# Performance work log

Measured on AMD Instinct MI355X. Metric: run time of the kernel, lower is better.

The kernel has to match this reference:

```python
import jax, jax.numpy as jnp
import numpy as np

N, E, G = 50000, 300000, 256
H, LAT, VOCAB = 256, 64, 100
BN_EPS = 1e-5


def _bn(x, gamma, beta):
    # BatchNorm1d in training mode: per-feature batch mean / biased var
    mu = x.mean(axis=0)
    var = x.var(axis=0)
    return gamma * (x - mu) * jax.lax.rsqrt(var + BN_EPS) + beta


def _gconv(x, edge_attr, src, dst):
    # message: softplus(x_j + e), aggregate: scatter-add to dst, update: +(1+eps)*x with eps=0
    m = jax.nn.softplus(x[src] + edge_attr)          # [E, H]
    agg = jax.ops.segment_sum(m, dst, num_segments=N)  # [N, H]
    return agg + x


def setup_inputs() -> dict:
    key = jax.random.key(0)
    ks = jax.random.split(key, 16)
    inp = {
        "node_type": jax.random.randint(ks[0], (N,), 0, VOCAB),
        "edge_type": jax.random.randint(ks[1], (E,), 0, VOCAB),
        "edge_index": jax.random.randint(ks[2], (2, E), 0, N),
        "batch": jnp.sort(jax.random.randint(ks[3], (N,), 0, G)),
        "node_emb_w": jax.random.normal(ks[4], (VOCAB, H), jnp.float32),
        "edge_emb_w": jax.random.normal(ks[5], (VOCAB, H), jnp.float32),
        "g1": jnp.ones((H,), jnp.float32), "b1": jnp.zeros((H,), jnp.float32),
        "g2": jnp.ones((H,), jnp.float32), "b2": jnp.zeros((H,), jnp.float32),
        "g3": jnp.ones((H,), jnp.float32), "b3": jnp.zeros((H,), jnp.float32),
        "go1": jnp.ones((H,), jnp.float32), "bo1": jnp.zeros((H,), jnp.float32),
        "go2": jnp.ones((H // 2,), jnp.float32), "bo2": jnp.zeros((H // 2,), jnp.float32),
        "W1": jax.random.normal(ks[6], (2 * H, H), jnp.float32) * (2 * H) ** -0.5,
        "B1": jnp.zeros((H,), jnp.float32),
        "W2": jax.random.normal(ks[7], (H, H // 2), jnp.float32) * H ** -0.5,
        "B2": jnp.zeros((H // 2,), jnp.float32),
        "W3": jax.random.normal(ks[8], (H // 2, 2 * LAT), jnp.float32) * (H // 2) ** -0.5,
        "B3": jnp.zeros((2 * LAT,), jnp.float32),
    }
    return inp


def reference(node_type, edge_type, edge_index, batch,
              node_emb_w, edge_emb_w,
              g1, b1, g2, b2, g3, b3, go1, bo1, go2, bo2,
              W1, B1, W2, B2, W3, B3):
    act = jax.nn.softplus
    src, dst = edge_index[0], edge_index[1]
    h = node_emb_w[node_type]            # [N, H]
    e = edge_emb_w[edge_type]            # [E, H]
    h = act(_bn(_gconv(h, e, src, dst), g1, b1))
    h = act(_bn(_gconv(h, e, src, dst), g2, b2))
    h = _bn(_gconv(h, e, src, dst), g3, b3)
    h_global = jax.ops.segment_sum(h, batch, num_segments=G)  # [G, H]
    feat = jnp.concatenate([h, h_global[batch]], axis=-1)     # [N, 2H]
    feat = act(_bn(feat @ W1 + B1, go1, bo1))
    feat = act(_bn(feat @ W2 + B2, go2, bo2))
    out = feat @ W3 + B3                                      # [N, 2*LAT]
    return out[:, :LAT], out[:, LAT:]
```

## Files before the change

kernel.cpp:

```cpp
#include <hip/hip_runtime.h>
#include <hip/hip_bf16.h>

namespace {

constexpr int N = 50000;
constexpr int E = 300000;
constexpr int G = 256;
constexpr int H = 256;
constexpr float EPS = 1e-5f;
constexpr int NB = (N + 255) / 256;
constexpr int POOL_S = 16;
constexpr int GBL = 256;
constexpr int NVB = N / 16;
constexpr float LOG2E = 1.4426950408889634f;
constexpr float LN2   = 0.6931471805599453f;

typedef unsigned short u16;
typedef __attribute__((ext_vector_type(8))) short bf16x8;
typedef __attribute__((ext_vector_type(4))) float f32x4;

__device__ __forceinline__ float expnabs(float z){
  float r; asm("v_exp_f32 %0, -abs(%1)" : "=v"(r) : "v"(z)); return r;
}
__device__ __forceinline__ float log2f_(float x){
  float r; asm("v_log_f32 %0, %1" : "=v"(r) : "v"(x)); return r;
}
__device__ __forceinline__ float spw(float zs){
  return fmaxf(zs, 0.f) + log2f_(1.f + expnabs(zs));
}
__device__ __forceinline__ u16 f2b(float f){
  union { float f; unsigned u; } v; v.f = f;
  unsigned r = v.u + 0x7FFF + ((v.u >> 16) & 1);
  return (u16)(r >> 16);
}
__device__ __forceinline__ float b2f(u16 u){
  union { unsigned i; float f; } v; v.i = ((unsigned)u) << 16; return v.f;
}
__device__ __forceinline__ float4 b2f4(ushort4 u){
  return make_float4(b2f(u.x), b2f(u.y), b2f(u.z), b2f(u.w));
}
__device__ __forceinline__ ushort4 f2b4(float4 v){
  ushort4 o; o.x = f2b(v.x); o.y = f2b(v.y); o.z = f2b(v.z); o.w = f2b(v.w);
  return o;
}

__global__ void k_pre(const int* __restrict__ nt, const float* __restrict__ nemb,
                      u16* __restrict__ xb, const int* __restrict__ dst,
                      int* __restrict__ cnt,
                      const float* __restrict__ W1, const float* __restrict__ W2,
                      const float* __restrict__ W3, const float* __restrict__ eemb,
                      u16* __restrict__ Wt1, u16* __restrict__ Wt2,
                      u16* __restrict__ Wt3, float* __restrict__ eembF){
  int idx = blockIdx.x * 256 + threadIdx.x;
  if (idx < N * 64){
    int i = idx >> 6, fq = (idx & 63) << 2;
    float4 v = *(const float4*)(nemb + (size_t)nt[i] * H + fq);
    v.x *= LOG2E; v.y *= LOG2E; v.z *= LOG2E; v.w *= LOG2E;
    *(ushort4*)(xb + (size_t)i * H + fq) = f2b4(v);
    return;
  }
  int j = idx - N * 64;
  if (j < E){ atomicAdd(&cnt[dst[j]], 1); return; }
  j -= E;
  if (j < 65536){ int c = j >> 8, k = j & 255; Wt1[j] = f2b(W1[(size_t)k * 256 + c]); return; }
  j -= 65536;
  if (j < 32768){ int c = j >> 8, k = j & 255; Wt2[j] = f2b(W2[(size_t)k * 128 + c]); return; }
  j -= 32768;
  if (j < 16384){ int c = j >> 7, k = j & 127; Wt3[j] = f2b(W3[(size_t)k * 128 + c]); return; }
  j -= 16384;
  if (j < 25600) eembF[j] = eemb[j] * LOG2E;
}

__global__ void k_scan1(const int* __restrict__ cnt, int* __restrict__ bsum){
  __shared__ int s[256];
  int t = threadIdx.x;
  int i = blockIdx.x * 256 + t;
  s[t] = (i < N) ? cnt[i] : 0;
  __syncthreads();
  for (int d = 128; d > 0; d >>= 1){
    if (t < d) s[t] += s[t + d];
    __syncthreads();
  }
  if (t == 0) bsum[blockIdx.x] = s[0];
}

__global__ void k_scan2(const int* __restrict__ bsum, int* __restrict__ bbase){
  __shared__ int s[256];
  int t = threadIdx.x;
  int orig = (t < NB) ? bsum[t] : 0;
  s[t] = orig;
  __syncthreads();
  for (int d = 1; d < 256; d <<= 1){
    int v = (t >= d) ? s[t - d] : 0;
    __syncthreads();
    s[t] += v;
    __syncthreads();
  }
  bbase[t] = s[t] - orig;
}

__global__ void k_scan3(const int* __restrict__ cnt, const int* __restrict__ bbase,
                        int* __restrict__ off, int* __restrict__ cur){
  __shared__ int s[256];
  int t = threadIdx.x;
  int i = blockIdx.x * 256 + t;
  int v = (i < N) ? cnt[i] : 0;
  s[t] = v;
  __syncthreads();
  for (int d = 1; d < 256; d <<= 1){
    int u = (t >= d) ? s[t - d] : 0;
    __syncthreads();
    s[t] += u;
    __syncthreads();
  }
  int excl = bbase[blockIdx.x] + s[t] - v;
  if (i < N){ off[i] = excl; cur[i] = excl; }
  if (i == N - 1) off[N] = excl + v;
}

__global__ void k_fill(const int* __restrict__ src, const int* __restrict__ dst,
                       const int* __restrict__ et, int* __restrict__ cur,
                       int2* __restrict__ edges_s){
  int e = blockIdx.x * 256 + threadIdx.x;
  if (e >= E) return;
  int d = dst[e];
  int p = atomicAdd(&cur[d], 1);
  edges_s[p] = make_int2(src[e] << 9, et[e] << 10);
}

__device__ __forceinline__ void acc_w(float4& acc, const float4 xs, const float4 es){
  acc.x += spw(xs.x + es.x);
  acc.y += spw(xs.y + es.y);
  acc.z += spw(xs.z + es.z);
  acc.w += spw(xs.w + es.w);
}

__global__ __launch_bounds__(1024)
void k_gather(const u16* __restrict__ xb, u16* __restrict__ agg,
              const int2* __restrict__ edges_s, const int* __restrict__ off,
              const float* __restrict__ eembF,
              float* __restrict__ sums, float* __restrict__ sumsq){
  __shared__ __align__(16) float elds[25600];
  __shared__ float reds[1024][4];
  __shared__ float reds2[1024][4];
  int tid = threadIdx.x;
  int w = tid >> 6, lane = tid & 63;
  int fx = lane << 3, fe = lane << 4;
  const char* xB = (const char*)xb;
  const char* eL = (const char*)elds;

  {
    const float4* s4 = (const float4*)eembF;
    float4* d4 = (float4*)elds;
    for (int t = tid; t < 6400; t += 1024) d4[t] = s4[t];
  }
  __syncthreads();

  float4 ls = make_float4(0.f, 0.f, 0.f, 0.f);
  float4 ls2 = make_float4(0.f, 0.f, 0.f, 0.f);
  for (int vb = blockIdx.x; vb < NVB; vb += GBL){
    int i = vb * 16 + w;
    float4 acc = b2f4(*(const ushort4*)(xB + ((size_t)i << 9) + fx));
    int lo = off[i], hi = off[i + 1];
    int j = lo;
    for (; j + 4 <= hi; j += 4){
      int2 s0 = edges_s[j + 0];
      int2 s1 = edges_s[j + 1];
      int2 s2 = edges_s[j + 2];
      int2 s3 = edges_s[j + 3];
      ushort4 x0 = *(const ushort4*)(xB + s0.x + fx);
      ushort4 x1 = *(const ushort4*)(xB + s1.x + fx);
      ushort4 x2 = *(const ushort4*)(xB + s2.x + fx);
      ushort4 x3 = *(const ushort4*)(xB + s3.x + fx);
      float4 e0 = *(const float4*)(eL + s0.y + fe);
      float4 e1 = *(const float4*)(eL + s1.y + fe);
      float4 e2 = *(const float4*)(eL + s2.y + fe);
      float4 e3 = *(const float4*)(eL + s3.y + fe);
      acc_w(acc, b2f4(x0), e0);
      acc_w(acc, b2f4(x1), e1);
      acc_w(acc, b2f4(x2), e2);
      acc_w(acc, b2f4(x3), e3);
    }
    if (j + 2 <= hi){
      int2 s0 = edges_s[j + 0];
      int2 s1 = edges_s[j + 1];
      ushort4 x0 = *(const ushort4*)(xB + s0.x + fx);
      ushort4 x1 = *(const ushort4*)(xB + s1.x + fx);
      float4 e0 = *(const float4*)(eL + s0.y + fe);
      float4 e1 = *(const float4*)(eL + s1.y + fe);
      acc_w(acc, b2f4(x0), e0);
      acc_w(acc, b2f4(x1), e1);
      j += 2;
    }
    if (j < hi){
      int2 s0 = edges_s[j];
      ushort4 x0 = *(const ushort4*)(xB + s0.x + fx);
      float4 e0 = *(const float4*)(eL + s0.y + fe);
      acc_w(acc, b2f4(x0), e0);
    }
    acc.x *= LN2; acc.y *= LN2; acc.z *= LN2; acc.w *= LN2;
    ls.x += acc.x; ls.y += acc.y; ls.z += acc.z; ls.w += acc.w;
    ls2.x += acc.x * acc.x; ls2.y += acc.y * acc.y;
    ls2.z += acc.z * acc.z; ls2.w += acc.w * acc.w;
    *(ushort4*)((char*)agg + ((size_t)i << 9) + fx) = f2b4(acc);
  }
  reds[tid][0] = ls.x;  reds[tid][1] = ls.y;  reds[tid][2] = ls.z;  reds[tid][3] = ls.w;
  reds2[tid][0] = ls2.x; reds2[tid][1] = ls2.y; reds2[tid][2] = ls2.z; reds2[tid][3] = ls2.w;
  __syncthreads();
  if (tid < 256){
    int f = tid;
    float ts = 0.f, ts2 = 0.f;
    #pragma unroll
    for (int w2 = 0; w2 < 16; ++w2){
      int s = w2 * 64 + (f >> 2);
      ts += reds[s][f & 3];
      ts2 += reds2[s][f & 3];
    }
    atomicAdd(&sums[f], ts);
    atomicAdd(&sumsq[f], ts2);
  }
}

template<int ACT, int SCALED>
__global__ void k_norm(const u16* __restrict__ in, u16* __restrict__ outb,
                       const float* __restrict__ sums, const float* __restrict__ sumsq,
                       const float* __restrict__ gamma, const float* __restrict__ beta,
                       int n4, int fmask){
  int idx = blockIdx.x * 256 + threadIdx.x;
  if (idx >= n4) return;
  int base = idx << 2;
  int f = base & fmask;
  float4 s = *(const float4*)(sums + f);
  float4 q = *(const float4*)(sumsq + f);
  float4 g = *(const float4*)(gamma + f);
  float4 bt = *(const float4*)(beta + f);
  float4 v = b2f4(*(const ushort4*)(in + base));
  const float inv = 1.f / N;
  float m, var, a, c;
  m = s.x * inv; var = q.x * inv - m * m; a = g.x * rsqrtf(var + EPS); c = bt.x - m * a; v.x = a * v.x + c;
  m = s.y * inv; var = q.y * inv - m * m; a = g.y * rsqrtf(var + EPS); c = bt.y - m * a; v.y = a * v.y + c;
  m = s.z * inv; var = q.z * inv - m * m; a = g.z * rsqrtf(var + EPS); c = bt.z - m * a; v.z = a * v.z + c;
  m = s.w * inv; var = q.w * inv - m * m; a = g.w * rsqrtf(var + EPS); c = bt.w - m * a; v.w = a * v.w + c;
  if (ACT){
    v.x = spw(v.x * LOG2E); v.y = spw(v.y * LOG2E);
    v.z = spw(v.z * LOG2E); v.w = spw(v.w * LOG2E);
    if (!SCALED){ v.x *= LN2; v.y *= LN2; v.z *= LN2; v.w *= LN2; }
  }
  *(ushort4*)(outb + base) = f2b4(v);
}

__global__ void k_pool_seg(const u16* __restrict__ xb, const int* __restrict__ batch,
                           float* __restrict__ hg){
  int g = blockIdx.x, sl = blockIdx.y;
  int f = threadIdx.x;
  int lo = 0, hi = N;
  while (lo < hi){ int m = (lo + hi) >> 1; if (batch[m] < g) lo = m + 1; else hi = m; }
  int start = lo;
  lo = 0; hi = N;
  while (lo < hi){ int m = (lo + hi) >> 1; if (batch[m] < g + 1) lo = m + 1; else hi = m; }
  int end = lo;
  int len = end - start;
  int a = start + (int)((long)len * sl / POOL_S);
  int b = start + (int)((long)len * (sl + 1) / POOL_S);
  if (a >= b) return;
  float s = 0.f;
  for (int i = a; i < b; ++i) s += b2f(xb[(size_t)i * H + f]);
  atomicAdd(&hg[g * H + f], s);
}

__global__ void k_hgw(const float* __restrict__ hg, const float* __restrict__ W1,
                      const float* __restrict__ B1, float* __restrict__ hgW){
  int g = blockIdx.x, c = threadIdx.x;
  float acc = B1[c];
  for (int k = 0; k < H; ++k)
    acc += hg[g * H + k] * W1[(size_t)(H + k) * H + c];
  hgW[g * H + c] = acc;
}

template<int K, int NC, int MODE, int WR, int STATS>
__global__ void k_mgemm(const u16* __restrict__ Ab, const u16* __restrict__ Wt,
                        const float* __restrict__ epi, const int* __restrict__ batch,
                        u16* __restrict__ outb, float* __restrict__ outf,
                        float* __restrict__ sums, float* __restrict__ sumsq){
  __shared__ float reds[256][4];
  __shared__ float reds2[256][4];
  constexpr int WC = 4 / WR;
  int tid = threadIdx.x;
  int w = tid >> 6, lane = tid & 63;
  int quad = lane >> 4, l15 = lane & 15;
  int wr = w / WC, wc = w % WC;
  int rowBase = blockIdx.x * (WR * 64) + wr * 64;
  int colBase = wc * 64;
  const u16* arow[4];
  #pragma unroll
  for (int t = 0; t < 4; ++t){
    int am = rowBase + t * 16 + l15;
    if (am >= N) am = N - 1;
    arow[t] = Ab + (size_t)am * K + quad * 8;
  }
  const u16* brow[4];
  #pragma unroll
  for (int u = 0; u < 4; ++u)
    brow[u] = Wt + (size_t)(colBase + u * 16 + l15) * K + quad * 8;
  f32x4 acc[4][4] = {};
  for (int k0 = 0; k0 < K; k0 += 32){
    bf16x8 a[4], b[4];
    #pragma unroll
    for (int t = 0; t < 4; ++t) a[t] = *(const bf16x8*)(arow[t] + k0);
    #pragma unroll
    for (int u = 0; u < 4; ++u) b[u] = *(const bf16x8*)(brow[u] + k0);
    #pragma unroll
    for (int t = 0; t < 4; ++t)
      #pragma unroll
      for (int u = 0; u < 4; ++u)
        acc[t][u] = __builtin_amdgcn_mfma_f32_16x16x32_bf16(a[t], b[u], acc[t][u], 0, 0, 0);
  }
  float ls[4] = {0.f, 0.f, 0.f, 0.f};
  float ls2[4] = {0.f, 0.f, 0.f, 0.f};
  #pragma unroll
  for (int t = 0; t < 4; ++t){
    #pragma unroll
    for (int r = 0; r < 4; ++r){
      int row = rowBase + t * 16 + quad * 4 + r;
      if (row >= N) continue;
      int g = (MODE == 0) ? batch[row] : 0;
      #pragma unroll
      for (int u = 0; u < 4; ++u){
        int n = colBase + u * 16 + l15;
        float v = acc[t][u][r];
        if (MODE == 0){
          v += epi[(size_t)g * NC + n];
          outb[(size_t)row * NC + n] = f2b(v);
        } else if (MODE == 1){
          v += epi[n];
          outb[(size_t)row * NC + n] = f2b(v);
        } else {
          v += epi[n];
          if (n < 64) outf[(size_t)row * 64 + n] = v;
          else        outf[(size_t)N * 64 + (size_t)row * 64 + (n - 64)] = v;
        }
        if (STATS){ ls[u] += v; ls2[u] += v * v; }
      }
    }
  }
  if (STATS){
    #pragma unroll
    for (int u = 0; u < 4; ++u){ reds[tid][u] = ls[u]; reds2[tid][u] = ls2[u]; }
    __syncthreads();
    int f = tid;
    if (f < NC){
      int fl = f & 15, fu = (f >> 4) & 3, fw = f >> 6;
      float ts = 0.f, ts2 = 0.f;
      if (WR == 1){
        #pragma unroll
        for (int q = 0; q < 4; ++q){
          int s = fw * 64 + q * 16 + fl;
          ts += reds[s][fu]; ts2 += reds2[s][fu];
        }
      } else {
        #pragma unroll
        for (int r2 = 0; r2 < 2; ++r2)
          #pragma unroll
          for (int q = 0; q < 4; ++q){
            int s = (r2 * 2 + fw) * 64 + q * 16 + fl;
            ts += reds[s][fu]; ts2 += reds2[s][fu];
          }
      }
      atomicAdd(&sums[f], ts);
      atomicAdd(&sumsq[f], ts2);
    }
  }
}

}

extern "C" void kernel_launch(void* const* d_in, const int* in_sizes, int n_in,
                              void* d_out, int out_size, void* d_ws, size_t ws_size,
                              hipStream_t stream){
  const int* node_type = (const int*)d_in[0];
  const int* edge_type = (const int*)d_in[1];
  const int* src       = (const int*)d_in[2];
  const int* dst       = src + E;
  const int* batch     = (const int*)d_in[3];
  const float* nemb = (const float*)d_in[4];
  const float* eemb = (const float*)d_in[5];
  const float* gs[3] = {(const float*)d_in[6], (const float*)d_in[8], (const float*)d_in[10]};
  const float* bs[3] = {(const float*)d_in[7], (const float*)d_in[9], (const float*)d_in[11]};
  const float* go1 = (const float*)d_in[12]; const float* bo1 = (const float*)d_in[13];
  const float* go2 = (const float*)d_in[14]; const float* bo2 = (const float*)d_in[15];
  const float* W1 = (const float*)d_in[16]; const float* B1 = (const float*)d_in[17];
  const float* W2 = (const float*)d_in[18]; const float* B2 = (const float*)d_in[19];
  const float* W3 = (const float*)d_in[20]; const float* B3 = (const float*)d_in[21];
  float* outf = (float*)d_out;

  char* p = (char*)d_ws;
  int*   cnt    = (int*)p;              p += (size_t)N * 4;
  float* hg     = (float*)p;            p += (size_t)G * H * 4;
  float* statsA = (float*)p;            p += 5 * 512 * 4;
  size_t zeroBytes = (size_t)p - (size_t)d_ws;
  float* hgW    = (float*)p;            p += (size_t)G * H * 4;
  int*   off    = (int*)p;              p += (size_t)(N + 1) * 4;
  int*   cur    = (int*)p;              p += (size_t)N * 4;
  int*   bsum   = (int*)p;              p += 256 * 4;
  int*   bbase  = (int*)p;              p += 256 * 4;
  int2*  edges_s= (int2*)p;             p += (size_t)E * 8;
  u16*   xb     = (u16*)p;              p += (size_t)N * H * 2;
  u16*   agg    = (u16*)p;              p += (size_t)N * H * 2;
  u16*   xf     = (u16*)p;              p += (size_t)N * 128 * 2;
  u16*   Wt1    = (u16*)p;              p += 65536 * 2;
  u16*   Wt2    = (u16*)p;              p += 32768 * 2;
  u16*   Wt3    = (u16*)p;              p += 16384 * 2;
  float* eembF  = (float*)p;            p += 25600 * 4;
  float* sumsL[5], *sumsqL[5];
  for (int k = 0; k < 5; ++k){ sumsL[k] = statsA + k * 512; sumsqL[k] = statsA + k * 512 + 256; }

  hipMemsetAsync(d_ws, 0, zeroBytes, stream);

  const int preItems = N * 64 + E + 65536 + 32768 + 16384 + 25600;
  k_pre<<<(preItems + 255) / 256, 256, 0, stream>>>(
      node_type, nemb, xb, dst, cnt, W1, W2, W3, eemb, Wt1, Wt2, Wt3, eembF);
  k_scan1<<<NB, 256, 0, stream>>>(cnt, bsum);
  k_scan2<<<1, 256, 0, stream>>>(bsum, bbase);
  k_scan3<<<NB, 256, 0, stream>>>(cnt, bbase, off, cur);
  k_fill<<<(E + 255) / 256, 256, 0, stream>>>(src, dst, edge_type, cur, edges_s);

  for (int l = 0; l < 3; ++l){
    k_gather<<<GBL, 1024, 0, stream>>>(xb, agg, edges_s, off, eembF, sumsL[l], sumsqL[l]);
    if (l < 2)
      k_norm<1, 1><<<(N * 64 + 255) / 256, 256, 0, stream>>>(
          agg, xb, sumsL[l], sumsqL[l], gs[l], bs[l], N * 64, 255);
    else
      k_norm<0, 0><<<(N * 64 + 255) / 256, 256, 0, stream>>>(
          agg, xb, sumsL[l], sumsqL[l], gs[l], bs[l], N * 64, 255);
  }

  {
    dim3 pg(G, POOL_S);
    k_pool_seg<<<pg, H, 0, stream>>>(xb, batch, hg);
  }
  k_hgw<<<G, H, 0, stream>>>(hg, W1, B1, hgW);

  k_mgemm<256, 256, 0, 1, 1><<<(N + 63) / 64, 256, 0, stream>>>(
      xb, Wt1, hgW, batch, agg, nullptr, sumsL[3], sumsqL[3]);
  k_norm<1, 0><<<(N * 64 + 255) / 256, 256, 0, stream>>>(
      agg, xb, sumsL[3], sumsqL[3], go1, bo1, N * 64, 255);

  k_mgemm<256, 128, 1, 2, 1><<<(N + 127) / 128, 256, 0, stream>>>(
      xb, Wt2, B2, nullptr, xf, nullptr, sumsL[4], sumsqL[4]);
  k_norm<1, 0><<<(N * 32 + 255) / 256, 256, 0, stream>>>(
      xf, xb, sumsL[4], sumsqL[4], go2, bo2, N * 32, 127);

  k_mgemm<128, 128, 2, 2, 0><<<(N + 127) / 128, 256, 0, stream>>>(
      xb, Wt3, B3, nullptr, nullptr, outf, nullptr, nullptr);
}
```

Baseline: 481.3 us.

## Stage MFMA GEMM tiles through LDS with async double-buffered loads

Rewrites the dense MFMA GEMM so each 256-thread block computes a 128x128 output tile. A and B slices of 64 K-columns are copied straight into LDS with global_load_lds, using an XOR swizzle and double buffering, replacing per-wave direct global reads of bf16 rows. The first GEMM's 256 output columns are split over a second grid dimension, and the column statistics are offset by the tile. The aim is to reuse loaded data across waves and overlap loads with MFMA, at the cost of two barriers per K step and out-of-range row reads on the last row block.

```diff
diff --git a/kernel.cpp b/kernel.cpp
--- a/kernel.cpp
+++ b/kernel.cpp
@@ -42,6 +42,12 @@
 __device__ __forceinline__ ushort4 f2b4(float4 v){
   ushort4 o; o.x = f2b(v.x); o.y = f2b(v.y); o.z = f2b(v.z); o.w = f2b(v.w);
   return o;
+}
+
+__device__ __forceinline__ void gl_lds16(const u16* g, u16* l){
+  __builtin_amdgcn_global_load_lds(
+      (const __attribute__((address_space(1))) unsigned int*)g,
+      (__attribute__((address_space(3))) unsigned int*)l, 16, 0, 0);
 }
 
 __global__ void k_pre(const int* __restrict__ nt, const float* __restrict__ nemb,
@@ -277,44 +283,68 @@
   hgW[g * H + c] = acc;
 }
 
-template<int K, int NC, int MODE, int WR, int STATS>
-__global__ void k_mgemm(const u16* __restrict__ Ab, const u16* __restrict__ Wt,
-                        const float* __restrict__ epi, const int* __restrict__ batch,
-                        u16* __restrict__ outb, float* __restrict__ outf,
-                        float* __restrict__ sums, float* __restrict__ sumsq){
-  __shared__ float reds[256][4];
-  __shared__ float reds2[256][4];
-  constexpr int WC = 4 / WR;
+template<int K, int NCOUT, int MODE, int STATS>
+__global__ __launch_bounds__(256)
+void k_mgemm(const u16* __restrict__ Ab, const u16* __restrict__ Wt,
+             const float* __restrict__ epi, const int* __restrict__ batch,
+             u16* __restrict__ outb, float* __restrict__ outf,
+             float* __restrict__ sums, float* __restrict__ sumsq){
+  constexpr int T = K / 64;
+  __shared__ __align__(16) u16 smem[32768];
   int tid = threadIdx.x;
   int w = tid >> 6, lane = tid & 63;
   int quad = lane >> 4, l15 = lane & 15;
-  int wr = w / WC, wc = w % WC;
-  int rowBase = blockIdx.x * (WR * 64) + wr * 64;
-  int colBase = wc * 64;
-  const u16* arow[4];
-  #pragma unroll
-  for (int t = 0; t < 4; ++t){
-    int am = rowBase + t * 16 + l15;
-    if (am >= N) am = N - 1;
-    arow[t] = Ab + (size_t)am * K + quad * 8;
-  }
-  const u16* brow[4];
-  #pragma unroll
-  for (int u = 0; u < 4; ++u)
-    brow[u] = Wt + (size_t)(colBase + u * 16 + l15) * K + quad * 8;
+  int wr = w >> 1, wc = w & 1;
+  int rowBase = blockIdx.x * 128 + wr * 64;
+  int colTile = blockIdx.y * 128;
+  const u16* Ag = Ab + (size_t)blockIdx.x * 128 * K;
+  const u16* Bg = Wt + (size_t)colTile * K;
+
+  int w6 = tid & 192;
+  auto stage = [&](const u16* gbase, u16* lbuf){
+    #pragma unroll
+    for (int it = 0; it < 4; ++it){
+      int p = it * 256 + tid;
+      int row = p >> 3, slot = p & 7;
+      const u16* g = gbase + (size_t)row * K + ((slot ^ (row & 7)) << 3);
+      gl_lds16(g, smem + ((size_t)((lbuf - smem) + (((it * 256 + w6)) << 3))));
+    }
+  };
+
+  stage(Ag, smem);
+  stage(Bg, smem + 16384);
+
   f32x4 acc[4][4] = {};
-  for (int k0 = 0; k0 < K; k0 += 32){
-    bf16x8 a[4], b[4];
+  int xb7 = l15 & 7;
+  for (int tt = 0; tt < T; ++tt){
+    if (tt + 1 < T){
+      int nb = (tt + 1) & 1;
+      stage(Ag + (tt + 1) * 64, smem + nb * 8192);
+      stage(Bg + (tt + 1) * 64, smem + 16384 + nb * 8192);
+    }
+    __syncthreads();
+    const u16* lA = smem + (tt & 1) * 8192;
+    const u16* lB = smem + 16384 + (tt & 1) * 8192;
     #pragma unroll
-    for (int t = 0; t < 4; ++t) a[t] = *(const bf16x8*)(arow[t] + k0);
-    #pragma unroll
-    for (int u = 0; u < 4; ++u) b[u] = *(const bf16x8*)(brow[u] + k0);
-    #pragma unroll
-    for (int t = 0; t < 4; ++t)
+    for (int ks = 0; ks < 2; ++ks){
+      int xs = (((ks << 2) | quad) ^ xb7) << 3;
+      bf16x8 a[4], b[4];
+      #pragma unroll
+      for (int t = 0; t < 4; ++t)
+        a[t] = *(const bf16x8*)(lA + ((wr * 64 + t * 16 + l15) << 6) + xs);
       #pragma unroll
       for (int u = 0; u < 4; ++u)
-        acc[t][u] = __builtin_amdgcn_mfma_f32_16x16x32_bf16(a[t], b[u], acc[t][u], 0, 0, 0);
-  }
+        b[u] = *(const bf16x8*)(lB + ((wc * 64 + u * 16 + l15) << 6) + xs);
+      #pragma unroll
+      for (int t = 0; t < 4; ++t)
+        #pragma unroll
+        for (int u = 0; u < 4; ++u)
+          acc[t][u] = __builtin_amdgcn_mfma_f32_16x16x32_bf16(a[t], b[u], acc[t][u], 0, 0, 0);
+    }
+    __syncthreads();
+  }
+
+  int colBase = colTile + wc * 64;
   float ls[4] = {0.f, 0.f, 0.f, 0.f};
   float ls2[4] = {0.f, 0.f, 0.f, 0.f};
   #pragma unroll
@@ -329,11 +359,11 @@
         int n = colBase + u * 16 + l15;
         float v = acc[t][u][r];
         if (MODE == 0){
-          v += epi[(size_t)g * NC + n];
-          outb[(size_t)row * NC + n] = f2b(v);
+          v += epi[(size_t)g * NCOUT + n];
+          outb[(size_t)row * NCOUT + n] = f2b(v);
         } else if (MODE == 1){
           v += epi[n];
-          outb[(size_t)row * NC + n] = f2b(v);
+          outb[(size_t)row * NCOUT + n] = f2b(v);
         } else {
           v += epi[n];
           if (n < 64) outf[(size_t)row * 64 + n] = v;
@@ -344,30 +374,24 @@
     }
   }
   if (STATS){
+    float (*reds)[4]  = (float (*)[4])smem;
+    float (*reds2)[4] = (float (*)[4])(smem + 2048);
     #pragma unroll
     for (int u = 0; u < 4; ++u){ reds[tid][u] = ls[u]; reds2[tid][u] = ls2[u]; }
     __syncthreads();
     int f = tid;
-    if (f < NC){
+    if (f < 128){
       int fl = f & 15, fu = (f >> 4) & 3, fw = f >> 6;
       float ts = 0.f, ts2 = 0.f;
-      if (WR == 1){
+      #pragma unroll
+      for (int r2 = 0; r2 < 2; ++r2)
         #pragma unroll
         for (int q = 0; q < 4; ++q){
-          int s = fw * 64 + q * 16 + fl;
+          int s = (r2 * 2 + fw) * 64 + q * 16 + fl;
           ts += reds[s][fu]; ts2 += reds2[s][fu];
         }
-      } else {
-        #pragma unroll
-        for (int r2 = 0; r2 < 2; ++r2)
-          #pragma unroll
-          for (int q = 0; q < 4; ++q){
-            int s = (r2 * 2 + fw) * 64 + q * 16 + fl;
-            ts += reds[s][fu]; ts2 += reds2[s][fu];
-          }
-      }
-      atomicAdd(&sums[f], ts);
-      atomicAdd(&sumsq[f], ts2);
+      atomicAdd(&sums[colTile + f], ts);
+      atomicAdd(&sumsq[colTile + f], ts2);
     }
   }
 }
@@ -440,16 +464,18 @@
   }
   k_hgw<<<G, H, 0, stream>>>(hg, W1, B1, hgW);
 
-  k_mgemm<256, 256, 0, 1, 1><<<(N + 63) / 64, 256, 0, stream>>>(
+  const int RB = (N + 127) / 128;
+
+  k_mgemm<256, 256, 0, 1><<<dim3(RB, 2), 256, 0, stream>>>(
       xb, Wt1, hgW, batch, agg, nullptr, sumsL[3], sumsqL[3]);
   k_norm<1, 0><<<(N * 64 + 255) / 256, 256, 0, stream>>>(
       agg, xb, sumsL[3], sumsqL[3], go1, bo1, N * 64, 255);
 
-  k_mgemm<256, 128, 1, 2, 1><<<(N + 127) / 128, 256, 0, stream>>>(
+  k_mgemm<256, 128, 1, 1><<<dim3(RB, 1), 256, 0, stream>>>(
       xb, Wt2, B2, nullptr, xf, nullptr, sumsL[4], sumsqL[4]);
   k_norm<1, 0><<<(N * 32 + 255) / 256, 256, 0, stream>>>(
       xf, xb, sumsL[4], sumsqL[4], go2, bo2, N * 32, 127);
 
-  k_mgemm<128, 128, 2, 2, 0><<<(N + 127) / 128, 256, 0, stream>>>(
+  k_mgemm<128, 128, 2, 0><<<dim3(RB, 1), 256, 0, stream>>>(
       xb, Wt3, B3, nullptr, nullptr, outf, nullptr, nullptr);
 }
```

After: 455.0 us, median of 2. 5.5% less time.
